# Kernel tuning notes

Measured on AMD Instinct MI355X. Metric: run time of the kernel, lower is better.

The kernel has to match this reference:

```python
import jax, jax.numpy as jnp
import numpy as np

N_NODES = 50000
N_EDGES = 800000
D_IN = 128
D_OUT = 128
BN_EPS = 1e-5


def setup_inputs() -> dict:
    key = jax.random.key(0)
    ks = jax.random.split(key, 8)
    node_feats = jax.random.normal(ks[0], (N_NODES, D_IN), dtype=jnp.float32)
    src = jax.random.randint(ks[1], (N_EDGES,), 0, N_NODES, dtype=jnp.int32)
    dst = jax.random.randint(ks[2], (N_EDGES,), 0, N_NODES, dtype=jnp.int32)
    # Glorot-ish init for weights
    scale = 1.0 / np.sqrt(D_IN)
    W = jax.random.normal(ks[3], (D_IN, D_OUT), dtype=jnp.float32) * scale
    b = jnp.zeros((D_OUT,), dtype=jnp.float32)
    Wr = jax.random.normal(ks[4], (D_IN, D_OUT), dtype=jnp.float32) * scale
    br = jnp.zeros((D_OUT,), dtype=jnp.float32)
    gamma = jnp.ones((D_OUT,), dtype=jnp.float32)
    beta = jnp.zeros((D_OUT,), dtype=jnp.float32)
    return {"node_feats": node_feats, "src": src, "dst": dst, "W": W, "b": b,
            "Wr": Wr, "br": br, "gamma": gamma, "beta": beta}


def reference(node_feats, src, dst, W, b, Wr, br, gamma, beta):
    N = node_feats.shape[0]
    ones_e = jnp.ones(src.shape[0], dtype=node_feats.dtype)
    # DGL GraphConv norm='both': D_out^{-1/2} on source side, D_in^{-1/2} on dest side
    deg_out = jnp.clip(jax.ops.segment_sum(ones_e, src, num_segments=N), 1.0)
    deg_in = jnp.clip(jax.ops.segment_sum(ones_e, dst, num_segments=N), 1.0)
    h = node_feats * jax.lax.rsqrt(deg_out)[:, None]        # [N, D_in]
    agg = jax.ops.segment_sum(h[src], dst, num_segments=N)  # gather + scatter-add, [N, D_in]
    agg = agg * jax.lax.rsqrt(deg_in)[:, None]
    gcn = jax.nn.relu(agg @ W + b)                           # GraphConv activation=relu
    res = jax.nn.relu(node_feats @ Wr + br)                  # residual branch
    y = gcn + res
    # BatchNorm1d (training mode: biased batch stats)
    mean = jnp.mean(y, axis=0)
    var = jnp.mean(jnp.square(y - mean), axis=0)
    out = (y - mean) * jax.lax.rsqrt(var + BN_EPS) * gamma + beta
    return out
```

## Files before the change

### kernel.cpp

```cpp
#include <hip/hip_runtime.h>

#define N_NODES 50000
#define N_EDGES 800000
#define D 128
#define BN_EPS 1e-5f
#define AGG_BLOCKS 2048
#define SCAN_BLOCKS 196
#define CHUNKS 64
#define EPC (N_EDGES / CHUNKS)
#define HALF_BINS 25600
#define HALF_U32 12800

typedef short bf16x8 __attribute__((ext_vector_type(8)));
typedef float f32x4  __attribute__((ext_vector_type(4)));
typedef float f32x2  __attribute__((ext_vector_type(2)));
typedef unsigned int u32x4 __attribute__((ext_vector_type(4)));


__device__ __forceinline__ unsigned int pack_rne(float a, float b) {
    unsigned int ua = __float_as_uint(a); ua += 0x7fffu + ((ua >> 16) & 1u);
    unsigned int ub = __float_as_uint(b); ub += 0x7fffu + ((ub >> 16) & 1u);
    return (ua >> 16) | (ub & 0xffff0000u);
}
__device__ __forceinline__ unsigned short pack1_rne(float a) {
    unsigned int ua = __float_as_uint(a); ua += 0x7fffu + ((ua >> 16) & 1u);
    return (unsigned short)(ua >> 16);
}
__device__ __forceinline__ unsigned char pack1_fp8(float a) {
    unsigned int u = __builtin_amdgcn_cvt_pk_fp8_f32(a, a, 0, false);
    return (unsigned char)(u & 0xffu);
}

__global__ __launch_bounds__(256) void hist_kernel(
        const int* __restrict__ dst, const int* __restrict__ src,
        unsigned int* __restrict__ histD, unsigned int* __restrict__ histS,
        const float* __restrict__ W, const float* __restrict__ Wr,
        uint4* __restrict__ pW, uint4* __restrict__ pWr) {
    __shared__ unsigned int h[HALF_U32];
    int tid = threadIdx.x;
    int c = blockIdx.x, r = blockIdx.y;
    if (c >= CHUNKS) {
        if (r != 0 || blockIdx.z != 0) return;
        int t = (c - CHUNKS) * 256 + tid;
        const float* S = (t & 2048) ? Wr : W;
        uint4* Dst     = (t & 2048) ? pWr : pW;
        int e = t & 2047;
        int lane = e & 63, ks = (e >> 6) & 3, ct = e >> 8;
        int n  = ct * 16 + (lane & 15);
        int k0 = ks * 32 + (lane >> 4) * 8;
        float v[8];
        #pragma unroll
        for (int j = 0; j < 8; j++) v[j] = S[(k0 + j) * D + n];
        uint4 rr;
        rr.x = pack_rne(v[0], v[1]); rr.y = pack_rne(v[2], v[3]);
        rr.z = pack_rne(v[4], v[5]); rr.w = pack_rne(v[6], v[7]);
        Dst[e] = rr;
        return;
    }
    const int* keys = blockIdx.z ? src : dst;
    unsigned int* hist = blockIdx.z ? histS : histD;
    for (int j = tid; j < HALF_U32; j += 256) h[j] = 0u;
    __syncthreads();
    int base = c * EPC;
    int lo = r * HALF_BINS;
    for (int i = tid; i < EPC; i += 256) {
        int b = keys[base + i] - lo;
        if ((unsigned)b < (unsigned)HALF_BINS)
            atomicAdd(&h[b >> 1], 1u << ((b & 1) * 16));
    }
    __syncthreads();
    unsigned int* out = hist + ((size_t)(r * CHUNKS + c)) * HALF_U32;
    for (int j = tid; j < HALF_U32; j += 256) out[j] = h[j];
}

__global__ __launch_bounds__(256) void merge_kernel(
        unsigned int* __restrict__ histD, unsigned int* __restrict__ histS,
        int* __restrict__ cnt_in, int* __restrict__ cnt_out) {
    int q = blockIdx.x * 256 + threadIdx.x;
    int r = blockIdx.y;
    unsigned int* hist = blockIdx.z ? histS : histD;
    int* cnt = blockIdx.z ? cnt_out : cnt_in;
    unsigned int lo = 0, hi = 0;
    for (int c = 0; c < CHUNKS; c++) {
        size_t idx = ((size_t)(r * CHUNKS + c)) * HALF_U32 + q;
        unsigned int v = hist[idx];
        hist[idx] = lo | (hi << 16);
        lo += v & 0xffffu; hi += v >> 16;
    }
    int n0 = r * HALF_BINS + q * 2;
    cnt[n0]     = (int)lo;
    cnt[n0 + 1] = (int)hi;
}

__global__ __launch_bounds__(256) void scan1_kernel(
        const int* __restrict__ cnt_in, int* __restrict__ row_ptr, int* __restrict__ blk_sum) {
    __shared__ int sh[256];
    int t = threadIdx.x;
    int i = blockIdx.x * 256 + t;
    int v = cnt_in[i];
    sh[t] = v;
    __syncthreads();
    int inc = v;
    #pragma unroll
    for (int off = 1; off < 256; off <<= 1) {
        int u = (t >= off) ? sh[t - off] : 0;
        __syncthreads();
        inc += u; sh[t] = inc;
        __syncthreads();
    }
    row_ptr[i] = inc - v;
    if (t == 255) blk_sum[blockIdx.x] = inc;
}

__global__ __launch_bounds__(256) void scan3_kernel(
        const int* __restrict__ cnt_in, const int* __restrict__ cnt_out,
        const int* __restrict__ blk_sum, int* __restrict__ row_ptr,
        float* __restrict__ rin, float* __restrict__ rout) {
    __shared__ int sh[256];
    int t = threadIdx.x;
    int v = (t < SCAN_BLOCKS) ? blk_sum[t] : 0;
    sh[t] = v;
    __syncthreads();
    int inc = v;
    #pragma unroll
    for (int off = 1; off < 256; off <<= 1) {
        int u = (t >= off) ? sh[t - off] : 0;
        __syncthreads();
        inc += u; sh[t] = inc;
        __syncthreads();
    }
    int boff = (blockIdx.x == 0) ? 0 : sh[blockIdx.x - 1];
    int i = blockIdx.x * 256 + t;
    if (i < N_NODES) {
        row_ptr[i] = row_ptr[i] + boff;
        int ci = cnt_in[i], co = cnt_out[i];
        rin[i]  = rsqrtf((float)(ci > 1 ? ci : 1));
        rout[i] = rsqrtf((float)(co > 1 ? co : 1));
    }
    if (blockIdx.x == SCAN_BLOCKS - 1 && t == 0) row_ptr[N_NODES] = N_EDGES;
}

__global__ __launch_bounds__(512) void fill2_kernel(
        const int* __restrict__ src, const int* __restrict__ dst,
        const int* __restrict__ row_ptr, const unsigned int* __restrict__ histP,
        int* __restrict__ csr_src) {
    __shared__ unsigned int h[HALF_U32];
    int tid = threadIdx.x;
    int c = blockIdx.x, r = blockIdx.y;
    int base = c * EPC;
    for (int j = tid; j < HALF_U32; j += 512) h[j] = 0u;
    __syncthreads();
    int lo = r * HALF_BINS;
    const unsigned int* pre_c = histP + ((size_t)(r * CHUNKS + c)) * HALF_U32;
    for (int i = tid; i < EPC; i += 512) {
        int d = dst[base + i];
        int b = d - lo;
        if ((unsigned)b < (unsigned)HALF_BINS) {
            int sh = (b & 1) * 16;
            unsigned int old = atomicAdd(&h[b >> 1], 1u << sh);
            unsigned int rank = (old >> sh) & 0xffffu;
            unsigned int pre = (pre_c[b >> 1] >> sh) & 0xffffu;
            int p = row_ptr[d] + (int)(pre + rank);
            csr_src[p] = src[base + i];
        }
    }
}

__global__ __launch_bounds__(256) void gemm_mfma(
        const float* __restrict__ x, const uint4* __restrict__ pW,
        const uint4* __restrict__ pWr, const float* __restrict__ br,
        const float* __restrict__ rout, unsigned char* __restrict__ hwb8,
        unsigned short* __restrict__ resb) {
    __shared__ unsigned short xs[64][136];
    int tid = threadIdx.x, wid = tid >> 6, lane = tid & 63;
    int quad = lane >> 4, l15 = lane & 15;
    int r0b = blockIdx.x * 64;
    const float4* xg = (const float4*)(x + (size_t)r0b * D);
    int maxidx = (N_NODES - r0b) * (D / 4);
    #pragma unroll
    for (int i = 0; i < 8; i++) {
        int idx = tid + 256 * i;
        float4 v = (idx < maxidx) ? xg[idx] : make_float4(0.f, 0.f, 0.f, 0.f);
        int row = idx >> 5, c0 = (idx & 31) * 4;
        *(unsigned int*)&xs[row][c0]     = pack_rne(v.x, v.y);
        *(unsigned int*)&xs[row][c0 + 2] = pack_rne(v.z, v.w);
    }
    __syncthreads();
    int wrow0 = wid * 16;
    bf16x8 A[4];
    #pragma unroll
    for (int ks = 0; ks < 4; ks++)
        A[ks] = *(const bf16x8*)&xs[wrow0 + l15][ks * 32 + quad * 8];
    f32x4 accW[8], accR[8];
    #pragma unroll
    for (int ct = 0; ct < 8; ct++) { accW[ct] = (f32x4)0.f; accR[ct] = (f32x4)0.f; }
    #pragma unroll
    for (int ct = 0; ct < 8; ct++) {
        #pragma unroll
        for (int ks = 0; ks < 4; ks++) {
            union { bf16x8 v; uint4 u; } Bw, Br2;
            Bw.u  = pW [(ct * 4 + ks) * 64 + lane];
            Br2.u = pWr[(ct * 4 + ks) * 64 + lane];
            accW[ct] = __builtin_amdgcn_mfma_f32_16x16x32_bf16(A[ks], Bw.v,  accW[ct], 0, 0, 0);
            accR[ct] = __builtin_amdgcn_mfma_f32_16x16x32_bf16(A[ks], Br2.v, accR[ct], 0, 0, 0);
        }
    }
    int r0 = r0b + wrow0;
    float ro[4]; int rowok[4];
    #pragma unroll
    for (int reg = 0; reg < 4; reg++) {
        int row = r0 + quad * 4 + reg;
        rowok[reg] = row < N_NODES;
        ro[reg] = rout[rowok[reg] ? row : N_NODES - 1];
    }
    #pragma unroll
    for (int ct = 0; ct < 8; ct++) {
        int c = ct * 16 + l15;
        float brv = br[c];
        #pragma unroll
        for (int reg = 0; reg < 4; reg++) {
            int row = r0 + quad * 4 + reg;
            if (rowok[reg]) {
                hwb8[(size_t)row * D + c] = pack1_fp8(accW[ct][reg] * ro[reg]);
                resb[(size_t)row * D + c] = pack1_rne(fmaxf(accR[ct][reg] + brv, 0.f));
            }
        }
    }
}

__device__ __forceinline__ float bf_lo(unsigned int v) { return __uint_as_float(v << 16); }
__device__ __forceinline__ float bf_hi(unsigned int v) { return __uint_as_float(v & 0xffff0000u); }

__device__ __forceinline__ void acc8f8(f32x2* a, const uint2 v) {
    a[0] += __builtin_amdgcn_cvt_pk_f32_fp8(v.x, false);
    a[1] += __builtin_amdgcn_cvt_pk_f32_fp8(v.x, true);
    a[2] += __builtin_amdgcn_cvt_pk_f32_fp8(v.y, false);
    a[3] += __builtin_amdgcn_cvt_pk_f32_fp8(v.y, true);
}
__device__ __forceinline__ void acc8f8m(f32x2* a, const uint2 v, float m) {
    f32x2 m2 = {m, m};
    a[0] += m2 * __builtin_amdgcn_cvt_pk_f32_fp8(v.x, false);
    a[1] += m2 * __builtin_amdgcn_cvt_pk_f32_fp8(v.x, true);
    a[2] += m2 * __builtin_amdgcn_cvt_pk_f32_fp8(v.y, false);
    a[3] += m2 * __builtin_amdgcn_cvt_pk_f32_fp8(v.y, true);
}

__device__ __forceinline__ void gather_accum(
        const unsigned char* __restrict__ hwb8, int myidx, int cnt,
        int qg, int ql, f32x2* a) {
    int i = 0;
    for (; i + 16 <= cnt; i += 16) {
        int p0 = __shfl(myidx, i + qg);
        int p1 = __shfl(myidx, i + 4 + qg);
        int p2 = __shfl(myidx, i + 8 + qg);
        int p3 = __shfl(myidx, i + 12 + qg);
        uint2 v0 = *((const uint2*)(hwb8 + (size_t)p0 * 128) + ql);
        uint2 v1 = *((const uint2*)(hwb8 + (size_t)p1 * 128) + ql);
        uint2 v2 = *((const uint2*)(hwb8 + (size_t)p2 * 128) + ql);
        uint2 v3 = *((const uint2*)(hwb8 + (size_t)p3 * 128) + ql);
        acc8f8(a, v0); acc8f8(a, v1); acc8f8(a, v2); acc8f8(a, v3);
    }
    for (; i + 4 <= cnt; i += 4) {
        int p0 = __shfl(myidx, i + qg);
        uint2 v0 = *((const uint2*)(hwb8 + (size_t)p0 * 128) + ql);
        acc8f8(a, v0);
    }
    int t = cnt - i;
    if (t > 0) {
        int j = i + qg; if (j > cnt - 1) j = cnt - 1;
        int p0 = __shfl(myidx, j);
        uint2 v0 = *((const uint2*)(hwb8 + (size_t)p0 * 128) + ql);
        float m = (qg < t) ? 1.f : 0.f;
        acc8f8m(a, v0, m);
    }
}

__global__ __launch_bounds__(256) void agg_kernel(
        const unsigned char* __restrict__ hwb8, const int* __restrict__ row_ptr,
        const int* __restrict__ csr_src, const float* __restrict__ rin,
        const float* __restrict__ bias, const unsigned short* __restrict__ resb,
        unsigned short* __restrict__ yb, float* __restrict__ parts) {
    __shared__ float red[4 * 256];
    int tid = threadIdx.x;
    int lane = tid & 63, wid = tid >> 6;
    int wave = blockIdx.x * 4 + wid;
    int nw = AGG_BLOCKS * 4;
    int qg = lane >> 4;
    int ql = lane & 15;
    float s1[8] = {0,0,0,0,0,0,0,0}, s2[8] = {0,0,0,0,0,0,0,0};
    float4 bv0, bv1;
    if (lane < 16) {
        bv0 = ((const float4*)bias)[2 * lane];
        bv1 = ((const float4*)bias)[2 * lane + 1];
    }
    int n = wave;
    int e0 = 0, e1 = 0, mi = 0;
    u32x4 rv4 = (u32x4)0u;
    float ri = 0.f;
    if (n < N_NODES) {
        e0 = row_ptr[n]; e1 = row_ptr[n + 1];
        ri = rin[n];
        if (lane < 16) rv4 = __builtin_nontemporal_load((const u32x4*)(resb + (size_t)n * D) + lane);
        int c0 = e1 - e0; if (c0 > 64) c0 = 64;
        mi = (lane < c0) ? __builtin_nontemporal_load(csr_src + e0 + lane) : 0;
    }
    while (n < N_NODES) {
        int nn = n + nw;
        int ne0 = 0, ne1 = 0, nmi = 0;
        u32x4 nrv = (u32x4)0u;
        float nri = 0.f;
        if (nn < N_NODES) {
            ne0 = row_ptr[nn]; ne1 = row_ptr[nn + 1];
            nri = rin[nn];
            if (lane < 16) nrv = __builtin_nontemporal_load((const u32x4*)(resb + (size_t)nn * D) + lane);
            int nc = ne1 - ne0; if (nc > 64) nc = 64;
            nmi = (lane < nc) ? __builtin_nontemporal_load(csr_src + ne0 + lane) : 0;
        }
        f32x2 av[4];
        av[0] = (f32x2)0.f; av[1] = (f32x2)0.f; av[2] = (f32x2)0.f; av[3] = (f32x2)0.f;
        {
            int cnt = e1 - e0; if (cnt > 64) cnt = 64;
            gather_accum(hwb8, mi, cnt, qg, ql, av);
        }
        for (int j0 = e0 + 64; j0 < e1; j0 += 64) {
            int cnt = e1 - j0; if (cnt > 64) cnt = 64;
            int mw = (lane < cnt) ? __builtin_nontemporal_load(csr_src + j0 + lane) : 0;
            gather_accum(hwb8, mw, cnt, qg, ql, av);
        }
        float a[8] = { av[0].x, av[0].y, av[1].x, av[1].y, av[2].x, av[2].y, av[3].x, av[3].y };
        #pragma unroll
        for (int k = 0; k < 8; k++) {
            a[k] += __shfl_xor(a[k], 16);
            a[k] += __shfl_xor(a[k], 32);
        }
        if (lane < 16) {
            float o[8];
            o[0] = fmaxf(a[0] * ri + bv0.x, 0.f) + bf_lo(rv4.x);
            o[1] = fmaxf(a[1] * ri + bv0.y, 0.f) + bf_hi(rv4.x);
            o[2] = fmaxf(a[2] * ri + bv0.z, 0.f) + bf_lo(rv4.y);
            o[3] = fmaxf(a[3] * ri + bv0.w, 0.f) + bf_hi(rv4.y);
            o[4] = fmaxf(a[4] * ri + bv1.x, 0.f) + bf_lo(rv4.z);
            o[5] = fmaxf(a[5] * ri + bv1.y, 0.f) + bf_hi(rv4.z);
            o[6] = fmaxf(a[6] * ri + bv1.z, 0.f) + bf_lo(rv4.w);
            o[7] = fmaxf(a[7] * ri + bv1.w, 0.f) + bf_hi(rv4.w);
            uint4 w;
            w.x = pack_rne(o[0], o[1]); w.y = pack_rne(o[2], o[3]);
            w.z = pack_rne(o[4], o[5]); w.w = pack_rne(o[6], o[7]);
            *((uint4*)(yb + (size_t)n * D) + lane) = w;
            #pragma unroll
            for (int k = 0; k < 8; k++) { s1[k] += o[k]; s2[k] += o[k] * o[k]; }
        }
        n = nn; e0 = ne0; e1 = ne1; mi = nmi; rv4 = nrv; ri = nri;
    }
    if (lane < 16) {
        int c0 = lane * 8;
        #pragma unroll
        for (int k = 0; k < 8; k++) {
            red[wid * 256 + c0 + k]       = s1[k];
            red[wid * 256 + 128 + c0 + k] = s2[k];
        }
    }
    __syncthreads();
    if (tid < 256) {
        float v = red[tid] + red[256 + tid] + red[512 + tid] + red[768 + tid];
        parts[(size_t)blockIdx.x * 256 + tid] = v;
    }
}

__global__ __launch_bounds__(256) void bn_fin2(
        const float* __restrict__ parts, const float* __restrict__ gamma,
        const float* __restrict__ beta, float* __restrict__ scsh) {
    __shared__ float rs1[256], rs2[256];
    int c = blockIdx.x, t = threadIdx.x;
    float s1 = 0.f, s2 = 0.f;
    for (int b = t; b < AGG_BLOCKS; b += 256) {
        s1 += parts[(size_t)b * 256 + c];
        s2 += parts[(size_t)b * 256 + 128 + c];
    }
    rs1[t] = s1; rs2[t] = s2;
    __syncthreads();
    for (int off = 128; off > 0; off >>= 1) {
        if (t < off) { rs1[t] += rs1[t + off]; rs2[t] += rs2[t + off]; }
        __syncthreads();
    }
    if (t == 0) {
        const float invN = 1.0f / (float)N_NODES;
        float mean = rs1[0] * invN;
        float var  = rs2[0] * invN - mean * mean;
        float sc = gamma[c] * rsqrtf(var + BN_EPS);
        scsh[c] = sc;
        scsh[128 + c] = beta[c] - mean * sc;
    }
}

__global__ void norm_kernel(const unsigned short* __restrict__ yb,
                            const float* __restrict__ scsh, float* __restrict__ out) {
    int i = blockIdx.x * blockDim.x + threadIdx.x;
    if (i < N_NODES * 16) {
        uint4 v = ((const uint4*)yb)[i];
        int c = (i & 15) * 8;
        f32x4 o0, o1;
        o0[0] = bf_lo(v.x) * scsh[c]     + scsh[128 + c];
        o0[1] = bf_hi(v.x) * scsh[c + 1] + scsh[128 + c + 1];
        o0[2] = bf_lo(v.y) * scsh[c + 2] + scsh[128 + c + 2];
        o0[3] = bf_hi(v.y) * scsh[c + 3] + scsh[128 + c + 3];
        o1[0] = bf_lo(v.z) * scsh[c + 4] + scsh[128 + c + 4];
        o1[1] = bf_hi(v.z) * scsh[c + 5] + scsh[128 + c + 5];
        o1[2] = bf_lo(v.w) * scsh[c + 6] + scsh[128 + c + 6];
        o1[3] = bf_hi(v.w) * scsh[c + 7] + scsh[128 + c + 7];
        f32x4* ov = (f32x4*)out + (size_t)i * 2;
        __builtin_nontemporal_store(o0, ov);
        __builtin_nontemporal_store(o1, ov + 1);
    }
}

extern "C" void kernel_launch(void* const* d_in, const int* in_sizes, int n_in,
                              void* d_out, int out_size, void* d_ws, size_t ws_size,
                              hipStream_t stream) {
    const float* x     = (const float*)d_in[0];
    const int*   src   = (const int*)d_in[1];
    const int*   dst   = (const int*)d_in[2];
    const float* W     = (const float*)d_in[3];
    const float* b     = (const float*)d_in[4];
    const float* Wr    = (const float*)d_in[5];
    const float* br    = (const float*)d_in[6];
    const float* gamma = (const float*)d_in[7];
    const float* beta  = (const float*)d_in[8];
    float* out = (float*)d_out;

    char* ws = (char*)d_ws;
    int*   cnt_in  = (int*)(ws + 0);
    int*   cnt_out = (int*)(ws + 262144);
    int*   row_ptr = (int*)(ws + 524288);
    float* rin     = (float*)(ws + 786432);
    float* rout    = (float*)(ws + 1048576);
    float* scsh    = (float*)(ws + 1310720);
    int*   blk_sum = (int*)(ws + 1312768);
    int*   csr_src = (int*)(ws + 1576960);
    unsigned char*  hwb8 = (unsigned char*)(ws + 4800000);
    unsigned short* resb = (unsigned short*)(ws + 11200000);
    unsigned short* yb   = (unsigned short*)(ws + 24000000);
    float* parts   = (float*)(ws + 36800000);
    uint4* pW      = (uint4*)(ws + 38897152);
    uint4* pWr     = (uint4*)(ws + 38929920);
    unsigned int* histD = (unsigned int*)(ws + 38962688);
    unsigned int* histS = (unsigned int*)(ws + 45516288);

    hist_kernel<<<dim3(CHUNKS + 16, 2, 2), 256, 0, stream>>>(dst, src, histD, histS, W, Wr, pW, pWr);
    merge_kernel<<<dim3(HALF_U32 / 256, 2, 2), 256, 0, stream>>>(histD, histS, cnt_in, cnt_out);
    scan1_kernel<<<SCAN_BLOCKS, 256, 0, stream>>>(cnt_in, row_ptr, blk_sum);
    scan3_kernel<<<SCAN_BLOCKS, 256, 0, stream>>>(cnt_in, cnt_out, blk_sum, row_ptr, rin, rout);
    fill2_kernel<<<dim3(CHUNKS, 2), 512, 0, stream>>>(src, dst, row_ptr, histD, csr_src);
    gemm_mfma<<<(N_NODES + 63) / 64, 256, 0, stream>>>(x, pW, pWr, br, rout, hwb8, resb);
    agg_kernel<<<AGG_BLOCKS, 256, 0, stream>>>(hwb8, row_ptr, csr_src, rin, b, resb, yb, parts);
    bn_fin2<<<128, 256, 0, stream>>>(parts, gamma, beta, scsh);
    norm_kernel<<<(N_NODES * 16 + 255) / 256, 256, 0, stream>>>(yb, scsh, out);
}
```

Before: 227.5 us.

## Fuse block scan into merge kernel, split fill into quarter bins, add nontemporal loads

The per-block exclusive scan of in-degree counts is folded into merge_kernel, which already holds the per-pair totals, so scan1_kernel and one launch disappear. scan3 now combines 100 block sums, each covering 512 nodes. fill2 is split into four bin ranges instead of two, halving its shared histogram and doubling its block count for more parallelism. Edge-index reads use nontemporal loads, at the cost of rereading dst more times in the fill pass.

```diff
diff --git a/kernel.cpp b/kernel.cpp
--- a/kernel.cpp
+++ b/kernel.cpp
@@ -10,6 +10,9 @@
 #define EPC (N_EDGES / CHUNKS)
 #define HALF_BINS 25600
 #define HALF_U32 12800
+#define QUART_BINS 12800
+#define QUART_U32 6400
+#define NB_MERGE 100
 
 typedef short bf16x8 __attribute__((ext_vector_type(8)));
 typedef float f32x4  __attribute__((ext_vector_type(4)));
@@ -64,7 +67,7 @@
     int base = c * EPC;
     int lo = r * HALF_BINS;
     for (int i = tid; i < EPC; i += 256) {
-        int b = keys[base + i] - lo;
+        int b = __builtin_nontemporal_load(keys + base + i) - lo;
         if ((unsigned)b < (unsigned)HALF_BINS)
             atomicAdd(&h[b >> 1], 1u << ((b & 1) * 16));
     }
@@ -75,8 +78,11 @@
 
 __global__ __launch_bounds__(256) void merge_kernel(
         unsigned int* __restrict__ histD, unsigned int* __restrict__ histS,
-        int* __restrict__ cnt_in, int* __restrict__ cnt_out) {
-    int q = blockIdx.x * 256 + threadIdx.x;
+        int* __restrict__ cnt_in, int* __restrict__ cnt_out,
+        int* __restrict__ row_ptr, int* __restrict__ blk_sum) {
+    __shared__ int sh[256];
+    int t = threadIdx.x;
+    int q = blockIdx.x * 256 + t;
     int r = blockIdx.y;
     unsigned int* hist = blockIdx.z ? histS : histD;
     int* cnt = blockIdx.z ? cnt_out : cnt_in;
@@ -90,17 +96,11 @@
     int n0 = r * HALF_BINS + q * 2;
     cnt[n0]     = (int)lo;
     cnt[n0 + 1] = (int)hi;
-}
-
-__global__ __launch_bounds__(256) void scan1_kernel(
-        const int* __restrict__ cnt_in, int* __restrict__ row_ptr, int* __restrict__ blk_sum) {
-    __shared__ int sh[256];
-    int t = threadIdx.x;
-    int i = blockIdx.x * 256 + t;
-    int v = cnt_in[i];
-    sh[t] = v;
-    __syncthreads();
-    int inc = v;
+    if (blockIdx.z) return;
+    int pair = (int)lo + (int)hi;
+    sh[t] = pair;
+    __syncthreads();
+    int inc = pair;
     #pragma unroll
     for (int off = 1; off < 256; off <<= 1) {
         int u = (t >= off) ? sh[t - off] : 0;
@@ -108,8 +108,10 @@
         inc += u; sh[t] = inc;
         __syncthreads();
     }
-    row_ptr[i] = inc - v;
-    if (t == 255) blk_sum[blockIdx.x] = inc;
+    int excl = inc - pair;
+    row_ptr[n0]     = excl;
+    row_ptr[n0 + 1] = excl + (int)lo;
+    if (t == 255) blk_sum[r * 50 + blockIdx.x] = inc;
 }
 
 __global__ __launch_bounds__(256) void scan3_kernel(
@@ -118,7 +120,7 @@
         float* __restrict__ rin, float* __restrict__ rout) {
     __shared__ int sh[256];
     int t = threadIdx.x;
-    int v = (t < SCAN_BLOCKS) ? blk_sum[t] : 0;
+    int v = (t < NB_MERGE) ? blk_sum[t] : 0;
     sh[t] = v;
     __syncthreads();
     int inc = v;
@@ -129,9 +131,10 @@
         inc += u; sh[t] = inc;
         __syncthreads();
     }
-    int boff = (blockIdx.x == 0) ? 0 : sh[blockIdx.x - 1];
     int i = blockIdx.x * 256 + t;
     if (i < N_NODES) {
+        int mb = i >> 9;
+        int boff = mb ? sh[mb - 1] : 0;
         row_ptr[i] = row_ptr[i] + boff;
         int ci = cnt_in[i], co = cnt_out[i];
         rin[i]  = rsqrtf((float)(ci > 1 ? ci : 1));
@@ -144,24 +147,26 @@
         const int* __restrict__ src, const int* __restrict__ dst,
         const int* __restrict__ row_ptr, const unsigned int* __restrict__ histP,
         int* __restrict__ csr_src) {
-    __shared__ unsigned int h[HALF_U32];
+    __shared__ unsigned int h[QUART_U32];
     int tid = threadIdx.x;
-    int c = blockIdx.x, r = blockIdx.y;
+    int c = blockIdx.x, s = blockIdx.y;
     int base = c * EPC;
-    for (int j = tid; j < HALF_U32; j += 512) h[j] = 0u;
-    __syncthreads();
-    int lo = r * HALF_BINS;
-    const unsigned int* pre_c = histP + ((size_t)(r * CHUNKS + c)) * HALF_U32;
+    for (int j = tid; j < QUART_U32; j += 512) h[j] = 0u;
+    __syncthreads();
+    int lo = s * QUART_BINS;
+    int r = s >> 1;
+    const unsigned int* pre_c = histP + ((size_t)(r * CHUNKS + c)) * HALF_U32
+                                      + (s & 1) * QUART_U32;
     for (int i = tid; i < EPC; i += 512) {
-        int d = dst[base + i];
+        int d = __builtin_nontemporal_load(dst + base + i);
         int b = d - lo;
-        if ((unsigned)b < (unsigned)HALF_BINS) {
-            int sh = (b & 1) * 16;
-            unsigned int old = atomicAdd(&h[b >> 1], 1u << sh);
-            unsigned int rank = (old >> sh) & 0xffffu;
-            unsigned int pre = (pre_c[b >> 1] >> sh) & 0xffffu;
+        if ((unsigned)b < (unsigned)QUART_BINS) {
+            int shft = (b & 1) * 16;
+            unsigned int old = atomicAdd(&h[b >> 1], 1u << shft);
+            unsigned int rank = (old >> shft) & 0xffffu;
+            unsigned int pre = (pre_c[b >> 1] >> shft) & 0xffffu;
             int p = row_ptr[d] + (int)(pre + rank);
-            csr_src[p] = src[base + i];
+            csr_src[p] = __builtin_nontemporal_load(src + base + i);
         }
     }
 }
@@ -447,10 +452,9 @@
     unsigned int* histS = (unsigned int*)(ws + 45516288);
 
     hist_kernel<<<dim3(CHUNKS + 16, 2, 2), 256, 0, stream>>>(dst, src, histD, histS, W, Wr, pW, pWr);
-    merge_kernel<<<dim3(HALF_U32 / 256, 2, 2), 256, 0, stream>>>(histD, histS, cnt_in, cnt_out);
-    scan1_kernel<<<SCAN_BLOCKS, 256, 0, stream>>>(cnt_in, row_ptr, blk_sum);
+    merge_kernel<<<dim3(HALF_U32 / 256, 2, 2), 256, 0, stream>>>(histD, histS, cnt_in, cnt_out, row_ptr, blk_sum);
     scan3_kernel<<<SCAN_BLOCKS, 256, 0, stream>>>(cnt_in, cnt_out, blk_sum, row_ptr, rin, rout);
-    fill2_kernel<<<dim3(CHUNKS, 2), 512, 0, stream>>>(src, dst, row_ptr, histD, csr_src);
+    fill2_kernel<<<dim3(CHUNKS, 4), 512, 0, stream>>>(src, dst, row_ptr, histD, csr_src);
     gemm_mfma<<<(N_NODES + 63) / 64, 256, 0, stream>>>(x, pW, pWr, br, rout, hwb8, resb);
     agg_kernel<<<AGG_BLOCKS, 256, 0, stream>>>(hwb8, row_ptr, csr_src, rin, b, resb, yb, parts);
     bn_fin2<<<128, 256, 0, stream>>>(parts, gamma, beta, scsh);
```

Measured after the change: 232.8 us. +2.3%, slower.

## Replace LDS histogram CSR build with global atomics and rank array, fuse fill into GEMM

Applied to the files above, without the earlier changes.

Replaces the chunked shared-memory histogram, merge and separate fill kernels with a single global-atomic counting pass that records each edge's per-destination rank. The CSR fill then becomes a plain scatter and is merged into the GEMM launch as extra blocks. The block-offset scan finish is recomputed locally in the consumers, and the degree rsqrt is computed inline, which removes the scan3 kernel and the rin/rout arrays. The aim is fewer kernel launches and less histogram traffic. In exchange it adds contended global atomics, a memset, and a redundant small scan in every agg and fill block; CSR order within a row is now nondeterministic.

```diff
diff --git a/kernel.cpp b/kernel.cpp
--- a/kernel.cpp
+++ b/kernel.cpp
@@ -6,10 +6,9 @@
 #define BN_EPS 1e-5f
 #define AGG_BLOCKS 2048
 #define SCAN_BLOCKS 196
-#define CHUNKS 64
-#define EPC (N_EDGES / CHUNKS)
-#define HALF_BINS 25600
-#define HALF_U32 12800
+#define NBLK_CNT 1024
+#define GEMM_BLKS 782
+#define FILL_BLKS 1024
 
 typedef short bf16x8 __attribute__((ext_vector_type(8)));
 typedef float f32x4  __attribute__((ext_vector_type(4)));
@@ -31,17 +30,15 @@
     return (unsigned char)(u & 0xffu);
 }
 
-__global__ __launch_bounds__(256) void hist_kernel(
-        const int* __restrict__ dst, const int* __restrict__ src,
-        unsigned int* __restrict__ histD, unsigned int* __restrict__ histS,
+__global__ __launch_bounds__(256) void count_kernel(
+        const int* __restrict__ src, const int* __restrict__ dst,
+        unsigned int* __restrict__ cnt_in, unsigned int* __restrict__ cnt_out,
+        unsigned short* __restrict__ rank16,
         const float* __restrict__ W, const float* __restrict__ Wr,
         uint4* __restrict__ pW, uint4* __restrict__ pWr) {
-    __shared__ unsigned int h[HALF_U32];
-    int tid = threadIdx.x;
-    int c = blockIdx.x, r = blockIdx.y;
-    if (c >= CHUNKS) {
-        if (r != 0 || blockIdx.z != 0) return;
-        int t = (c - CHUNKS) * 256 + tid;
+    int tid = threadIdx.x, bx = blockIdx.x;
+    if (bx >= NBLK_CNT) {
+        int t = (bx - NBLK_CNT) * 256 + tid;
         const float* S = (t & 2048) ? Wr : W;
         uint4* Dst     = (t & 2048) ? pWr : pW;
         int e = t & 2047;
@@ -57,47 +54,22 @@
         Dst[e] = rr;
         return;
     }
-    const int* keys = blockIdx.z ? src : dst;
-    unsigned int* hist = blockIdx.z ? histS : histD;
-    for (int j = tid; j < HALF_U32; j += 256) h[j] = 0u;
-    __syncthreads();
-    int base = c * EPC;
-    int lo = r * HALF_BINS;
-    for (int i = tid; i < EPC; i += 256) {
-        int b = keys[base + i] - lo;
-        if ((unsigned)b < (unsigned)HALF_BINS)
-            atomicAdd(&h[b >> 1], 1u << ((b & 1) * 16));
-    }
-    __syncthreads();
-    unsigned int* out = hist + ((size_t)(r * CHUNKS + c)) * HALF_U32;
-    for (int j = tid; j < HALF_U32; j += 256) out[j] = h[j];
-}
-
-__global__ __launch_bounds__(256) void merge_kernel(
-        unsigned int* __restrict__ histD, unsigned int* __restrict__ histS,
-        int* __restrict__ cnt_in, int* __restrict__ cnt_out) {
-    int q = blockIdx.x * 256 + threadIdx.x;
-    int r = blockIdx.y;
-    unsigned int* hist = blockIdx.z ? histS : histD;
-    int* cnt = blockIdx.z ? cnt_out : cnt_in;
-    unsigned int lo = 0, hi = 0;
-    for (int c = 0; c < CHUNKS; c++) {
-        size_t idx = ((size_t)(r * CHUNKS + c)) * HALF_U32 + q;
-        unsigned int v = hist[idx];
-        hist[idx] = lo | (hi << 16);
-        lo += v & 0xffffu; hi += v >> 16;
-    }
-    int n0 = r * HALF_BINS + q * 2;
-    cnt[n0]     = (int)lo;
-    cnt[n0 + 1] = (int)hi;
+    for (int e = bx * 256 + tid; e < N_EDGES; e += NBLK_CNT * 256) {
+        int d = __builtin_nontemporal_load(dst + e);
+        int s = __builtin_nontemporal_load(src + e);
+        unsigned int r = atomicAdd(&cnt_in[d], 1u);
+        atomicAdd(&cnt_out[s], 1u);
+        rank16[e] = (unsigned short)r;
+    }
 }
 
 __global__ __launch_bounds__(256) void scan1_kernel(
-        const int* __restrict__ cnt_in, int* __restrict__ row_ptr, int* __restrict__ blk_sum) {
+        const unsigned int* __restrict__ cnt_in, int* __restrict__ row_ptr,
+        int* __restrict__ blk_sum) {
     __shared__ int sh[256];
     int t = threadIdx.x;
     int i = blockIdx.x * 256 + t;
-    int v = cnt_in[i];
+    int v = (int)cnt_in[i];
     sh[t] = v;
     __syncthreads();
     int inc = v;
@@ -112,12 +84,8 @@
     if (t == 255) blk_sum[blockIdx.x] = inc;
 }
 
-__global__ __launch_bounds__(256) void scan3_kernel(
-        const int* __restrict__ cnt_in, const int* __restrict__ cnt_out,
-        const int* __restrict__ blk_sum, int* __restrict__ row_ptr,
-        float* __restrict__ rin, float* __restrict__ rout) {
-    __shared__ int sh[256];
-    int t = threadIdx.x;
+__device__ __forceinline__ void scan_blksum(const int* __restrict__ blk_sum,
+                                            int* sh, int t) {
     int v = (t < SCAN_BLOCKS) ? blk_sum[t] : 0;
     sh[t] = v;
     __syncthreads();
@@ -129,50 +97,33 @@
         inc += u; sh[t] = inc;
         __syncthreads();
     }
-    int boff = (blockIdx.x == 0) ? 0 : sh[blockIdx.x - 1];
-    int i = blockIdx.x * 256 + t;
-    if (i < N_NODES) {
-        row_ptr[i] = row_ptr[i] + boff;
-        int ci = cnt_in[i], co = cnt_out[i];
-        rin[i]  = rsqrtf((float)(ci > 1 ? ci : 1));
-        rout[i] = rsqrtf((float)(co > 1 ? co : 1));
-    }
-    if (blockIdx.x == SCAN_BLOCKS - 1 && t == 0) row_ptr[N_NODES] = N_EDGES;
-}
-
-__global__ __launch_bounds__(512) void fill2_kernel(
-        const int* __restrict__ src, const int* __restrict__ dst,
-        const int* __restrict__ row_ptr, const unsigned int* __restrict__ histP,
-        int* __restrict__ csr_src) {
-    __shared__ unsigned int h[HALF_U32];
-    int tid = threadIdx.x;
-    int c = blockIdx.x, r = blockIdx.y;
-    int base = c * EPC;
-    for (int j = tid; j < HALF_U32; j += 512) h[j] = 0u;
-    __syncthreads();
-    int lo = r * HALF_BINS;
-    const unsigned int* pre_c = histP + ((size_t)(r * CHUNKS + c)) * HALF_U32;
-    for (int i = tid; i < EPC; i += 512) {
-        int d = dst[base + i];
-        int b = d - lo;
-        if ((unsigned)b < (unsigned)HALF_BINS) {
-            int sh = (b & 1) * 16;
-            unsigned int old = atomicAdd(&h[b >> 1], 1u << sh);
-            unsigned int rank = (old >> sh) & 0xffffu;
-            unsigned int pre = (pre_c[b >> 1] >> sh) & 0xffffu;
-            int p = row_ptr[d] + (int)(pre + rank);
-            csr_src[p] = src[base + i];
-        }
-    }
-}
-
-__global__ __launch_bounds__(256) void gemm_mfma(
+}
+#define BLK_OFF(sh, mb) ((mb) ? (sh)[(mb) - 1] : 0)
+
+__global__ __launch_bounds__(256) void gemfill_kernel(
         const float* __restrict__ x, const uint4* __restrict__ pW,
         const uint4* __restrict__ pWr, const float* __restrict__ br,
-        const float* __restrict__ rout, unsigned char* __restrict__ hwb8,
-        unsigned short* __restrict__ resb) {
+        const unsigned int* __restrict__ cnt_out, unsigned char* __restrict__ hwb8,
+        unsigned short* __restrict__ resb,
+        const int* __restrict__ src, const int* __restrict__ dst,
+        const unsigned short* __restrict__ rank16, const int* __restrict__ row_ptr,
+        const int* __restrict__ blk_sum, int* __restrict__ csr_src) {
     __shared__ unsigned short xs[64][136];
-    int tid = threadIdx.x, wid = tid >> 6, lane = tid & 63;
+    __shared__ int sh[256];
+    int tid = threadIdx.x;
+    if (blockIdx.x >= GEMM_BLKS) {
+        scan_blksum(blk_sum, sh, tid);
+        int fb = blockIdx.x - GEMM_BLKS;
+        for (int e = fb * 256 + tid; e < N_EDGES; e += FILL_BLKS * 256) {
+            int d = __builtin_nontemporal_load(dst + e);
+            int s = __builtin_nontemporal_load(src + e);
+            int rk = (int)__builtin_nontemporal_load(rank16 + e);
+            int p = row_ptr[d] + BLK_OFF(sh, d >> 8) + rk;
+            csr_src[p] = s;
+        }
+        return;
+    }
+    int wid = tid >> 6, lane = tid & 63;
     int quad = lane >> 4, l15 = lane & 15;
     int r0b = blockIdx.x * 64;
     const float4* xg = (const float4*)(x + (size_t)r0b * D);
@@ -211,7 +162,8 @@
     for (int reg = 0; reg < 4; reg++) {
         int row = r0 + quad * 4 + reg;
         rowok[reg] = row < N_NODES;
-        ro[reg] = rout[rowok[reg] ? row : N_NODES - 1];
+        int cw = (int)cnt_out[rowok[reg] ? row : N_NODES - 1];
+        ro[reg] = rsqrtf((float)(cw > 1 ? cw : 1));
     }
     #pragma unroll
     for (int ct = 0; ct < 8; ct++) {
@@ -277,11 +229,14 @@
 
 __global__ __launch_bounds__(256) void agg_kernel(
         const unsigned char* __restrict__ hwb8, const int* __restrict__ row_ptr,
-        const int* __restrict__ csr_src, const float* __restrict__ rin,
+        const int* __restrict__ blk_sum, const unsigned int* __restrict__ cnt_in,
+        const int* __restrict__ csr_src,
         const float* __restrict__ bias, const unsigned short* __restrict__ resb,
         unsigned short* __restrict__ yb, float* __restrict__ parts) {
     __shared__ float red[4 * 256];
+    __shared__ int sho[256];
     int tid = threadIdx.x;
+    scan_blksum(blk_sum, sho, tid);
     int lane = tid & 63, wid = tid >> 6;
     int wave = blockIdx.x * 4 + wid;
     int nw = AGG_BLOCKS * 4;
@@ -298,8 +253,10 @@
     u32x4 rv4 = (u32x4)0u;
     float ri = 0.f;
     if (n < N_NODES) {
-        e0 = row_ptr[n]; e1 = row_ptr[n + 1];
-        ri = rin[n];
+        e0 = row_ptr[n] + BLK_OFF(sho, n >> 8);
+        e1 = row_ptr[n + 1] + BLK_OFF(sho, (n + 1) >> 8);
+        int ci = (int)cnt_in[n];
+        ri = rsqrtf((float)(ci > 1 ? ci : 1));
         if (lane < 16) rv4 = __builtin_nontemporal_load((const u32x4*)(resb + (size_t)n * D) + lane);
         int c0 = e1 - e0; if (c0 > 64) c0 = 64;
         mi = (lane < c0) ? __builtin_nontemporal_load(csr_src + e0 + lane) : 0;
@@ -310,8 +267,10 @@
         u32x4 nrv = (u32x4)0u;
         float nri = 0.f;
         if (nn < N_NODES) {
-            ne0 = row_ptr[nn]; ne1 = row_ptr[nn + 1];
-            nri = rin[nn];
+            ne0 = row_ptr[nn] + BLK_OFF(sho, nn >> 8);
+            ne1 = row_ptr[nn + 1] + BLK_OFF(sho, (nn + 1) >> 8);
+            int ci = (int)cnt_in[nn];
+            nri = rsqrtf((float)(ci > 1 ? ci : 1));
             if (lane < 16) nrv = __builtin_nontemporal_load((const u32x4*)(resb + (size_t)nn * D) + lane);
             int nc = ne1 - ne0; if (nc > 64) nc = 64;
             nmi = (lane < nc) ? __builtin_nontemporal_load(csr_src + ne0 + lane) : 0;
@@ -429,11 +388,9 @@
     float* out = (float*)d_out;
 
     char* ws = (char*)d_ws;
-    int*   cnt_in  = (int*)(ws + 0);
-    int*   cnt_out = (int*)(ws + 262144);
+    unsigned int* cnt_in  = (unsigned int*)(ws + 0);
+    unsigned int* cnt_out = (unsigned int*)(ws + 262144);
     int*   row_ptr = (int*)(ws + 524288);
-    float* rin     = (float*)(ws + 786432);
-    float* rout    = (float*)(ws + 1048576);
     float* scsh    = (float*)(ws + 1310720);
     int*   blk_sum = (int*)(ws + 1312768);
     int*   csr_src = (int*)(ws + 1576960);
@@ -443,16 +400,17 @@
     float* parts   = (float*)(ws + 36800000);
     uint4* pW      = (uint4*)(ws + 38897152);
     uint4* pWr     = (uint4*)(ws + 38929920);
-    unsigned int* histD = (unsigned int*)(ws + 38962688);
-    unsigned int* histS = (unsigned int*)(ws + 45516288);
-
-    hist_kernel<<<dim3(CHUNKS + 16, 2, 2), 256, 0, stream>>>(dst, src, histD, histS, W, Wr, pW, pWr);
-    merge_kernel<<<dim3(HALF_U32 / 256, 2, 2), 256, 0, stream>>>(histD, histS, cnt_in, cnt_out);
+    unsigned short* rank16 = (unsigned short*)(ws + 38962688);
+
+    hipMemsetAsync(ws, 0, 524288, stream);
+    count_kernel<<<NBLK_CNT + 16, 256, 0, stream>>>(src, dst, cnt_in, cnt_out,
+                                                    rank16, W, Wr, pW, pWr);
     scan1_kernel<<<SCAN_BLOCKS, 256, 0, stream>>>(cnt_in, row_ptr, blk_sum);
-    scan3_kernel<<<SCAN_BLOCKS, 256, 0, stream>>>(cnt_in, cnt_out, blk_sum, row_ptr, rin, rout);
-    fill2_kernel<<<dim3(CHUNKS, 2), 512, 0, stream>>>(src, dst, row_ptr, histD, csr_src);
-    gemm_mfma<<<(N_NODES + 63) / 64, 256, 0, stream>>>(x, pW, pWr, br, rout, hwb8, resb);
-    agg_kernel<<<AGG_BLOCKS, 256, 0, stream>>>(hwb8, row_ptr, csr_src, rin, b, resb, yb, parts);
+    gemfill_kernel<<<GEMM_BLKS + FILL_BLKS, 256, 0, stream>>>(
+        x, pW, pWr, br, cnt_out, hwb8, resb,
+        src, dst, rank16, row_ptr, blk_sum, csr_src);
+    agg_kernel<<<AGG_BLOCKS, 256, 0, stream>>>(hwb8, row_ptr, blk_sum, cnt_in,
+                                               csr_src, b, resb, yb, parts);
     bn_fin2<<<128, 256, 0, stream>>>(parts, gamma, beta, scsh);
     norm_kernel<<<(N_NODES * 16 + 255) / 256, 256, 0, stream>>>(yb, scsh, out);
 }
```

New measurement: 250.1 us. 9.9% more time.
